# Kernel optimization log

Measured on AMD Instinct MI355X. Metric: run time of the kernel, lower is better.

Reference implementation:

```python
import math
import jax, jax.numpy as jnp
import numpy as np

B, N, CS, CZ, CH, H, PQ, PV = 1, 4096, 512, 128, 64, 16, 4, 8
BQ, BK = 32, 128
NB = N // BQ
CZ4 = CZ // 4
INF = 100000.0
EPS = 1e-8


def quat_to_rot(q):
    w, x, y, z = q[..., 0], q[..., 1], q[..., 2], q[..., 3]
    return jnp.stack([
        jnp.stack([1 - 2 * (y * y + z * z), 2 * (x * y - w * z), 2 * (x * z + w * y)], -1),
        jnp.stack([2 * (x * y + w * z), 1 - 2 * (x * x + z * z), 2 * (y * z - w * x)], -1),
        jnp.stack([2 * (x * z - w * y), 2 * (y * z + w * x), 1 - 2 * (x * x + y * y)], -1),
    ], -2)


def setup_inputs() -> dict:
    key = jax.random.key(0)
    ks = jax.random.split(key, 16)
    s = jax.random.normal(ks[0], (B, N, CS), jnp.float32)
    z = jax.random.normal(ks[1], (B, NB, BQ, BK, CZ), jnp.float32)
    trans = jax.random.normal(ks[2], (B, N, 3), jnp.float32) * 10.0
    quat = jax.random.normal(ks[3], (B, N, 4), jnp.float32)
    quat = quat / jnp.linalg.norm(quat, axis=-1, keepdims=True)
    rots = quat_to_rot(quat)
    s_mask = jnp.ones((B, N), jnp.float32)
    pad = (BK - BQ) // 2  # key window centered on each query block
    key_idx = (jnp.arange(NB)[:, None] * BQ - pad + jnp.arange(BK)[None, :]).astype(jnp.int32)

    def w(k, shp):
        return jax.random.normal(k, shp, jnp.float32) * (1.0 / math.sqrt(shp[0]))

    return {
        's': s, 'z': z, 'trans': trans, 'rots': rots, 's_mask': s_mask, 'key_idx': key_idx,
        'Wq': w(ks[4], (CS, H * CH)), 'Wk': w(ks[5], (CS, H * CH)), 'Wv': w(ks[6], (CS, H * CH)),
        'Wqp': w(ks[7], (CS, H * PQ * 3)), 'Wkvp': w(ks[8], (CS, H * (PQ + PV) * 3)),
        'Wb': w(ks[9], (CZ, H)), 'Wdz': w(ks[10], (CZ, CZ4)),
        'head_weights': jnp.full((H,), float(np.log(np.e - 1.0)), jnp.float32),  # softplus^-1(1)
        'Wout': w(ks[11], (H * (CZ4 + CH + PV * 4), CS)),
        'g_s': jnp.ones((CS,), jnp.float32), 'b_s': jnp.zeros((CS,), jnp.float32),
        'g_z': jnp.ones((CZ,), jnp.float32), 'b_z': jnp.zeros((CZ,), jnp.float32),
    }


def _ln(x, g, b):
    m = jnp.mean(x, -1, keepdims=True)
    v = jnp.mean((x - m) ** 2, -1, keepdims=True)
    return (x - m) * jax.lax.rsqrt(v + 1e-5) * g + b


def _ipa(s, z, trans, rots, s_mask, key_idx, Wq, Wk, Wv, Wqp, Wkvp, Wb, Wdz,
         head_weights, Wout, g_s, b_s, g_z, b_z):
    s_n = _ln(s, g_s, b_s)
    z_n = _ln(z, g_z, b_z)

    valid = (key_idx >= 0) & (key_idx < N)            # [NB, BK]
    idx = jnp.clip(key_idx, 0, N - 1)
    vf = valid.astype(s.dtype)[None]                  # [1, NB, BK]

    def gk(x):  # gather key window: [B,N,...] -> [B,NB,BK,...]
        return x[:, idx]

    sq = s_n.reshape(B, NB, BQ, CS)
    sk = gk(s_n) * vf[..., None]                      # zero-pad out-of-range keys

    tq = trans.reshape(B, NB, BQ, 3)
    rq = rots.reshape(B, NB, BQ, 3, 3)
    tk = gk(trans) * vf[..., None]
    rk = jnp.where(valid[None, :, :, None, None], gk(rots), jnp.eye(3, dtype=rots.dtype))

    q = (sq @ Wq).reshape(B, NB, BQ, H, CH)
    k = (sk @ Wk).reshape(B, NB, BK, H, CH)
    v = (sk @ Wv).reshape(B, NB, BK, H, CH)

    q_pts = (sq @ Wqp).reshape(B, NB, BQ, H * PQ, 3)
    q_pts = jnp.einsum('bnqij,bnqpj->bnqpi', rq, q_pts) + tq[:, :, :, None, :]
    q_pts = q_pts.reshape(B, NB, BQ, H, PQ, 3)

    kv_pts = (sk @ Wkvp).reshape(B, NB, BK, H * (PQ + PV), 3)
    kv_pts = jnp.einsum('bnkij,bnkpj->bnkpi', rk, kv_pts) + tk[:, :, :, None, :]
    kv_pts = kv_pts.reshape(B, NB, BK, H, PQ + PV, 3)
    k_pts, v_pts = kv_pts[..., :PQ, :], kv_pts[..., PQ:, :]

    bias = jnp.einsum('bnqkc,ch->bnqkh', z_n, Wb)
    a = jnp.einsum('bnqhc,bnkhc->bnqkh', q, k) * math.sqrt(1.0 / (3 * CH))
    a = a + math.sqrt(1.0 / 3) * bias

    disp = q_pts[:, :, :, None] - k_pts[:, :, None]   # [B,NB,BQ,BK,H,PQ,3]
    pt_att = jnp.sum(disp ** 2, -1)                   # [B,NB,BQ,BK,H,PQ]
    hw = jax.nn.softplus(head_weights) * math.sqrt(1.0 / (3 * (PQ * 9.0 / 2)))
    pt_att = -0.5 * jnp.sum(pt_att * hw[:, None], -1)  # [B,NB,BQ,BK,H]

    qm = s_mask.reshape(B, NB, BQ)
    km = gk(s_mask) * vf
    amask = INF * (qm[:, :, :, None] * km[:, :, None, :] - 1.0)

    a = a + pt_att + amask[..., None]
    a = jax.nn.softmax(jnp.swapaxes(a, -1, -2), axis=-1)  # [B,NB,BQ,H,BK]

    o = jnp.einsum('bnqhk,bnkhc->bnqhc', a, v).reshape(B, NB, BQ, H * CH)

    o_pt = jnp.einsum('bnqhk,bnkhpc->bnqhpc', a, v_pts)
    o_pt = jnp.einsum('bnqji,bnqhpj->bnqhpi', rq, o_pt - tq[:, :, :, None, None, :])
    o_pt_norm = jnp.sqrt(jnp.sum(o_pt ** 2, -1) + EPS).reshape(B, NB, BQ, H * PV)
    o_pt = o_pt.reshape(B, NB, BQ, H * PV * 3)

    pair_z = z_n @ Wdz                                # [B,NB,BQ,BK,CZ4]
    o_pair = jnp.einsum('bnqhk,bnqkc->bnqhc', a, pair_z).reshape(B, NB, BQ, H * CZ4)

    out = jnp.concatenate([o, o_pt, o_pt_norm, o_pair], -1) @ Wout
    return out.reshape(B, N, CS)


def reference(s, z, trans, rots, s_mask, key_idx, Wq, Wk, Wv, Wqp, Wkvp, Wb, Wdz,
              head_weights, Wout, g_s, b_s, g_z, b_z):
    return _ipa(s, z, trans, rots, s_mask, key_idx, Wq, Wk, Wv, Wqp, Wkvp, Wb, Wdz,
                head_weights, Wout, g_s, b_s, g_z, b_z)
```

## Files before the change

kernel.cpp:

```cpp
#include <hip/hip_runtime.h>
#include <math.h>

#define D_N 4096
#define PBW 3072
#define PPW 768
#define OFFK 1024
#define OFFV 2048
#define CATW 2048

typedef __bf16 bf16_t;
typedef __bf16 bf16x8 __attribute__((ext_vector_type(8)));
typedef __bf16 bf16x4 __attribute__((ext_vector_type(4)));
typedef float f32x4 __attribute__((ext_vector_type(4)));

__device__ __forceinline__ void gld16(const void* g, void* l) {
    __builtin_amdgcn_global_load_lds((const __attribute__((address_space(1))) unsigned int*)g,
                                     (__attribute__((address_space(3))) unsigned int*)l, 16, 0, 0);
}

__global__ __launch_bounds__(256) void k_prep(
    const float* __restrict__ Wq, const float* __restrict__ Wk, const float* __restrict__ Wv,
    const float* __restrict__ Wqp, const float* __restrict__ Wkvp, const float* __restrict__ Wout,
    const float* __restrict__ Wb, const float* __restrict__ Wdz,
    const float* __restrict__ gz, const float* __restrict__ bz,
    const float* __restrict__ s, const float* __restrict__ g_s, const float* __restrict__ b_s,
    bf16_t* __restrict__ wcatT, bf16_t* __restrict__ WoutT,
    bf16_t* __restrict__ WzT, float* __restrict__ Kv, bf16_t* __restrict__ s_nb)
{
    __shared__ float T[64][65];
    const int bx = blockIdx.x;
    const int tid = threadIdx.x;
    if (bx < 736) {
        const float* src; int ld, coff, r0;
        bf16_t* dst; int Rdst;
        if (bx < 480) {
            int c0 = (bx % 60) * 64;
            r0 = (bx / 60) * 64;
            if (c0 < 1024)      { src = Wq;   ld = 1024; coff = c0; }
            else if (c0 < 2048) { src = Wk;   ld = 1024; coff = c0 - 1024; }
            else if (c0 < 3072) { src = Wv;   ld = 1024; coff = c0 - 2048; }
            else if (c0 < 3264) { src = Wqp;  ld = 192;  coff = c0 - 3072; }
            else                { src = Wkvp; ld = 576;  coff = c0 - 3264; }
            dst = wcatT + (size_t)c0 * 512; Rdst = 512;
        } else {
            int b = bx - 480;
            int c0 = (b & 7) * 64;
            r0 = (b >> 3) * 64;
            src = Wout; ld = 512; coff = c0;
            dst = WoutT + (size_t)c0 * 2048; Rdst = 2048;
        }
        {
            int rr = tid >> 2, cb = (tid & 3) * 16;
            const float* p = src + (size_t)(r0 + rr) * ld + coff + cb;
            #pragma unroll
            for (int i = 0; i < 4; ++i)
                *(float4*)&T[rr][cb + i * 4] = *(const float4*)(p + i * 4);
        }
        __syncthreads();
        {
            int cc = tid >> 2, rb = (tid & 3) * 16;
            bf16_t* o = dst + (size_t)cc * Rdst + r0 + rb;
            bf16x8 o0, o1;
            #pragma unroll
            for (int j = 0; j < 8; ++j) o0[j] = (bf16_t)T[rb + j][cc];
            #pragma unroll
            for (int j = 0; j < 8; ++j) o1[j] = (bf16_t)T[rb + 8 + j][cc];
            *(bf16x8*)(o) = o0;
            *(bf16x8*)(o + 8) = o1;
        }
    } else if (bx == 736) {
        for (int i = tid; i < 6144; i += 256) {
            int j = i >> 7, c = i & 127;
            float w = (j < 16) ? Wb[c * 16 + j] : Wdz[c * 32 + (j - 16)];
            WzT[i] = (bf16_t)(gz[c] * w);
        }
        if (tid < 48) {
            int j = tid;
            float acc = 0.f;
            for (int c = 0; c < 128; ++c) {
                float w = (j < 16) ? Wb[c * 16 + j] : Wdz[c * 32 + (j - 16)];
                acc += bz[c] * w;
            }
            Kv[j] = acc;
        }
    } else {
        int row = (bx - 737) * 4 + (tid >> 6);
        int lane = tid & 63;
        const float4* p = (const float4*)(s + (size_t)row * 512);
        float4 v0 = p[lane];
        float4 v1 = p[lane + 64];
        float sum = v0.x + v0.y + v0.z + v0.w + v1.x + v1.y + v1.z + v1.w;
        float sq  = v0.x*v0.x + v0.y*v0.y + v0.z*v0.z + v0.w*v0.w
                  + v1.x*v1.x + v1.y*v1.y + v1.z*v1.z + v1.w*v1.w;
        #pragma unroll
        for (int off = 1; off < 64; off <<= 1) {
            sum += __shfl_xor(sum, off);
            sq  += __shfl_xor(sq, off);
        }
        float m = sum * (1.0f / 512.0f);
        float var = sq * (1.0f / 512.0f) - m * m;
        float rs = rsqrtf(var + 1e-5f);
        int c = lane * 4;
        int c2 = 256 + lane * 4;
        bf16x4 r0, r1;
        r0[0] = (bf16_t)((v0.x - m) * rs * g_s[c+0] + b_s[c+0]);
        r0[1] = (bf16_t)((v0.y - m) * rs * g_s[c+1] + b_s[c+1]);
        r0[2] = (bf16_t)((v0.z - m) * rs * g_s[c+2] + b_s[c+2]);
        r0[3] = (bf16_t)((v0.w - m) * rs * g_s[c+3] + b_s[c+3]);
        r1[0] = (bf16_t)((v1.x - m) * rs * g_s[c2+0] + b_s[c2+0]);
        r1[1] = (bf16_t)((v1.y - m) * rs * g_s[c2+1] + b_s[c2+1]);
        r1[2] = (bf16_t)((v1.z - m) * rs * g_s[c2+2] + b_s[c2+2]);
        r1[3] = (bf16_t)((v1.w - m) * rs * g_s[c2+3] + b_s[c2+3]);
        *(bf16x4*)(s_nb + (size_t)row * 512 + c)  = r0;
        *(bf16x4*)(s_nb + (size_t)row * 512 + c2) = r1;
    }
}

__global__ __launch_bounds__(256) void k_fused(
    const bf16_t* __restrict__ A, const bf16_t* __restrict__ BT,
    bf16_t* __restrict__ projb, float* __restrict__ projp,
    const float* __restrict__ z, const bf16_t* __restrict__ WzT, const float* __restrict__ Kv,
    float* __restrict__ biasT, bf16_t* __restrict__ pzT)
{
    __shared__ __align__(16) char smem[65536];
    const int bx = blockIdx.x;
    const int tid = threadIdx.x, lane = tid & 63, w = tid >> 6;
    int gemm_id = -1, zid = 0;
    if (bx < 2880) {
        int s3 = bx % 3, b3 = bx / 3;
        if (s3 == 0) gemm_id = b3;
        else         zid = b3 * 2 + s3 - 1;
    } else {
        zid = 1920 + (bx - 2880);
    }

    if (gemm_id >= 0) {
        bf16_t (*Asl)[32] = (bf16_t(*)[32])smem;
        bf16_t (*Bsl)[32] = (bf16_t(*)[32])(smem + 8192);
        const int row0 = (gemm_id / 30) * 128, col0 = (gemm_id % 30) * 128;
        const int wr = (w >> 1) * 64, wc = (w & 1) * 64;
        const int K = 512;
        const int sr = lane >> 2, k8 = (lane & 3) * 8;
        const bf16_t* Ab = A + (size_t)(row0 + w * 32 + sr) * K + k8;
        const bf16_t* Bb = BT + (size_t)(col0 + w * 32 + sr) * K + k8;
        f32x4 acc[4][4];
        #pragma unroll
        for (int m = 0; m < 4; ++m)
            #pragma unroll
            for (int n = 0; n < 4; ++n) acc[m][n] = (f32x4){0.f,0.f,0.f,0.f};
        for (int k0 = 0; k0 < K; k0 += 32) {
            __syncthreads();
            gld16(Ab + k0,          &Asl[w * 32][0]);
            gld16(Ab + k0 + 16 * K, &Asl[w * 32 + 16][0]);
            gld16(Bb + k0,          &Bsl[w * 32][0]);
            gld16(Bb + k0 + 16 * K, &Bsl[w * 32 + 16][0]);
            __syncthreads();
            bf16x8 af[4], bfr[4];
            #pragma unroll
            for (int m = 0; m < 4; ++m) af[m]  = *(const bf16x8*)&Asl[wr + m*16 + (lane & 15)][(lane >> 4) * 8];
            #pragma unroll
            for (int n = 0; n < 4; ++n) bfr[n] = *(const bf16x8*)&Bsl[wc + n*16 + (lane & 15)][(lane >> 4) * 8];
            #pragma unroll
            for (int m = 0; m < 4; ++m)
                #pragma unroll
                for (int n = 0; n < 4; ++n)
                    acc[m][n] = __builtin_amdgcn_mfma_f32_16x16x32_bf16(af[m], bfr[n], acc[m][n], 0, 0, 0);
        }
        if (col0 < 3072) {
            #pragma unroll
            for (int m = 0; m < 4; ++m)
                #pragma unroll
                for (int n = 0; n < 4; ++n)
                    #pragma unroll
                    for (int i = 0; i < 4; ++i)
                        projb[(size_t)(row0 + wr + m*16 + (lane >> 4)*4 + i) * PBW + col0 + wc + n*16 + (lane & 15)]
                            = (bf16_t)acc[m][n][i];
        } else {
            #pragma unroll
            for (int m = 0; m < 4; ++m)
                #pragma unroll
                for (int n = 0; n < 4; ++n)
                    #pragma unroll
                    for (int i = 0; i < 4; ++i)
                        projp[(size_t)(row0 + wr + m*16 + (lane >> 4)*4 + i) * PPW + col0 - 3072 + wc + n*16 + (lane & 15)]
                            = acc[m][n][i];
        }
        return;
    }

    float (*zbuf)[64][128] = (float(*)[64][128])smem;
    const int r16 = lane & 15, kg = lane >> 4;
    bf16x8 bfz[3][4];
    #pragma unroll
    for (int nt = 0; nt < 3; ++nt)
        #pragma unroll
        for (int kc = 0; kc < 4; ++kc)
            bfz[nt][kc] = *(const bf16x8*)(WzT + (size_t)(nt * 16 + r16) * 128 + kc * 32 + kg * 8);
    float K0 = Kv[r16], K1 = Kv[16 + r16], K2 = Kv[32 + r16];
    asm volatile("s_waitcnt vmcnt(0)" ::: "memory");
    __builtin_amdgcn_sched_barrier(0);

    const int gid = zid * 4 + w;
    const char* zb = (const char*)z + (size_t)gid * 64 * 512;
    char* lb0 = (char*)&zbuf[0][w * 16][0];
    char* lb1 = (char*)&zbuf[1][w * 16][0];

#define STAGE(i, lb) { \
    const char* gp_ = zb + (size_t)(i) * 8192 + lane * 16; \
    _Pragma("unroll") \
    for (int c_ = 0; c_ < 8; ++c_) gld16(gp_ + c_ * 1024, (lb) + c_ * 1024); }

#define PROCESS(i, b) { \
    const float* rp = &zbuf[b][w * 16 + r16][kg * 8]; \
    float4 za[4], zc[4]; \
    float sum = 0.f, sq = 0.f; \
    _Pragma("unroll") \
    for (int kc = 0; kc < 4; ++kc) { \
        float4 a_ = *(const float4*)(rp + kc * 32); \
        float4 b_ = *(const float4*)(rp + kc * 32 + 4); \
        za[kc] = a_; zc[kc] = b_; \
        sum += a_.x + a_.y + a_.z + a_.w + b_.x + b_.y + b_.z + b_.w; \
        sq  += a_.x*a_.x + a_.y*a_.y + a_.z*a_.z + a_.w*a_.w + b_.x*b_.x + b_.y*b_.y + b_.z*b_.z + b_.w*b_.w; \
    } \
    sum += __shfl_xor(sum, 16); sq += __shfl_xor(sq, 16); \
    sum += __shfl_xor(sum, 32); sq += __shfl_xor(sq, 32); \
    float m_ = sum * (1.0f / 128.0f); \
    float rs_ = rsqrtf(sq * (1.0f / 128.0f) - m_ * m_ + 1e-5f); \
    bf16x8 af[4]; \
    _Pragma("unroll") \
    for (int kc = 0; kc < 4; ++kc) { \
        af[kc][0] = (bf16_t)((za[kc].x - m_) * rs_); \
        af[kc][1] = (bf16_t)((za[kc].y - m_) * rs_); \
        af[kc][2] = (bf16_t)((za[kc].z - m_) * rs_); \
        af[kc][3] = (bf16_t)((za[kc].w - m_) * rs_); \
        af[kc][4] = (bf16_t)((zc[kc].x - m_) * rs_); \
        af[kc][5] = (bf16_t)((zc[kc].y - m_) * rs_); \
        af[kc][6] = (bf16_t)((zc[kc].z - m_) * rs_); \
        af[kc][7] = (bf16_t)((zc[kc].w - m_) * rs_); \
    } \
    f32x4 acc0 = (f32x4){0.f,0.f,0.f,0.f}; \
    f32x4 acc1 = (f32x4){0.f,0.f,0.f,0.f}; \
    f32x4 acc2 = (f32x4){0.f,0.f,0.f,0.f}; \
    _Pragma("unroll") \
    for (int kc = 0; kc < 4; ++kc) { \
        acc0 = __builtin_amdgcn_mfma_f32_16x16x32_bf16(af[kc], bfz[0][kc], acc0, 0, 0, 0); \
        acc1 = __builtin_amdgcn_mfma_f32_16x16x32_bf16(af[kc], bfz[1][kc], acc1, 0, 0, 0); \
        acc2 = __builtin_amdgcn_mfma_f32_16x16x32_bf16(af[kc], bfz[2][kc], acc2, 0, 0, 0); \
    } \
    const int t_ = gid * 4 + (i); \
    const int rowq_ = t_ >> 3; \
    const int k0_ = ((t_ & 7) << 4) + kg * 4; \
    float4 bw = {acc0[0] + K0, acc0[1] + K0, acc0[2] + K0, acc0[3] + K0}; \
    *(float4*)&biasT[((size_t)rowq_ * 16 + r16) * 128 + k0_] = bw; \
    bf16x4 p1, p2; \
    _Pragma("unroll") \
    for (int i2 = 0; i2 < 4; ++i2) { p1[i2] = (bf16_t)(acc1[i2] + K1); p2[i2] = (bf16_t)(acc2[i2] + K2); } \
    *(bf16x4*)&pzT[((size_t)rowq_ * 32 + r16) * 128 + k0_] = p1; \
    *(bf16x4*)&pzT[((size_t)rowq_ * 32 + 16 + r16) * 128 + k0_] = p2; }

#define LDS_DRAIN asm volatile("s_waitcnt lgkmcnt(0)" ::: "memory"); __builtin_amdgcn_sched_barrier(0);

    STAGE(0, lb0);
    STAGE(1, lb1);
    asm volatile("s_waitcnt vmcnt(8)" ::: "memory");
    __builtin_amdgcn_sched_barrier(0);
    PROCESS(0, 0);
    LDS_DRAIN
    STAGE(2, lb0);
    asm volatile("s_waitcnt vmcnt(8)" ::: "memory");
    __builtin_amdgcn_sched_barrier(0);
    PROCESS(1, 1);
    LDS_DRAIN
    STAGE(3, lb1);
    asm volatile("s_waitcnt vmcnt(8)" ::: "memory");
    __builtin_amdgcn_sched_barrier(0);
    PROCESS(2, 0);
    asm volatile("s_waitcnt vmcnt(0)" ::: "memory");
    __builtin_amdgcn_sched_barrier(0);
    PROCESS(3, 1);
#undef STAGE
#undef PROCESS
#undef LDS_DRAIN
}

__global__ __launch_bounds__(256) void k_attn4(
    const bf16_t* __restrict__ projb, const float* __restrict__ projp,
    const float* __restrict__ biasT, const float* __restrict__ rots,
    const float* __restrict__ trans, const float* __restrict__ smask,
    const int* __restrict__ kidx, const float* __restrict__ hwraw,
    bf16_t* __restrict__ catb, bf16_t* __restrict__ Pbf)
{
    __shared__ __align__(16) char pool[51840];
    bf16_t (*Qs)[72]   = (bf16_t(*)[72])pool;
    bf16_t (*Ks)[72]   = (bf16_t(*)[72])(pool + 32 * 72 * 2);
    bf16_t (*Vt)[136]  = (bf16_t(*)[136])pool;
    float  (*att)[132] = (float(*)[132])(pool + 26112);
    bf16_t (*Ps)[136]  = (bf16_t(*)[136])(pool + 26112);
    float  (*optmp)[33]= (float(*)[33])(pool + 26112 + 8704);
    float  (*kp_s)[12] = (float(*)[12])(pool + 43008);
    float  (*qp_s)[12] = (float(*)[12])(pool + 49152);
    float*  km_s       = (float*)(pool + 50688);
    float*  qm_s       = (float*)(pool + 51200);
    int*    rows_s     = (int*)(pool + 51328);

    const int wgid = blockIdx.x;
    const int swz = (wgid & 7) * 256 + (wgid >> 3);
    const int h = swz >> 7;
    const int nblk = swz & 127;
    const int tid = threadIdx.x;
    const int lane = tid & 63;
    const int w = tid >> 6;
    const int rowq0 = nblk * 32;
    const float hw = log1pf(__expf(hwraw[h])) * 0.13608276348795434f;

    if (tid < 128) {
        int ki = kidx[nblk * 128 + tid];
        int valid = (ki >= 0 && ki < D_N);
        int rr = ki < 0 ? 0 : (ki > D_N - 1 ? D_N - 1 : ki);
        rows_s[tid] = rr;
        km_s[tid] = valid ? smask[rr] : 0.0f;
    } else if (tid < 160) {
        qm_s[tid - 128] = smask[rowq0 + tid - 128];
    }
    __syncthreads();
    {
        int q = tid >> 3, cg = (tid & 7) * 8;
        *(bf16x8*)&Qs[q][cg] = *(const bf16x8*)(projb + (size_t)(rowq0 + q) * PBW + h * 64 + cg);
    }
    float Rk[9], tk0 = 0.f, tk1 = 0.f, tk2 = 0.f;
    if (tid < 128) {
        int rr = rows_s[tid];
        const float* Rp = rots + (size_t)rr * 9;
        const float* tp = trans + (size_t)rr * 3;
        #pragma unroll
        for (int e = 0; e < 9; ++e) Rk[e] = Rp[e];
        tk0 = tp[0]; tk1 = tp[1]; tk2 = tp[2];
        const float* kp = projp + (size_t)rr * PPW + 192 + h * 36;
        float4 p0 = *(const float4*)kp;
        float4 p1 = *(const float4*)(kp + 4);
        float4 p2 = *(const float4*)(kp + 8);
        float xs[4] = {p0.x, p0.w, p1.z, p2.y};
        float ys[4] = {p0.y, p1.x, p1.w, p2.z};
        float zs[4] = {p0.z, p1.y, p2.x, p2.w};
        #pragma unroll
        for (int p = 0; p < 4; ++p) {
            kp_s[tid][p*3+0] = Rk[0]*xs[p] + Rk[1]*ys[p] + Rk[2]*zs[p] + tk0;
            kp_s[tid][p*3+1] = Rk[3]*xs[p] + Rk[4]*ys[p] + Rk[5]*zs[p] + tk1;
            kp_s[tid][p*3+2] = Rk[6]*xs[p] + Rk[7]*ys[p] + Rk[8]*zs[p] + tk2;
        }
    } else {
        int j = tid - 128;
        {
            int q = j >> 2, p = j & 3;
            const float* Rp = rots + (size_t)(rowq0 + q) * 9;
            const float* tp = trans + (size_t)(rowq0 + q) * 3;
            const float* qp = projp + (size_t)(rowq0 + q) * PPW + h * 12 + p * 3;
            float x = qp[0], y = qp[1], zc = qp[2];
            qp_s[q][p*3+0] = Rp[0]*x + Rp[1]*y + Rp[2]*zc + tp[0];
            qp_s[q][p*3+1] = Rp[3]*x + Rp[4]*y + Rp[5]*zc + tp[1];
            qp_s[q][p*3+2] = Rp[6]*x + Rp[7]*y + Rp[8]*zc + tp[2];
        }
        {
            const bf16_t* pK = projb + (size_t)rows_s[j] * PBW + OFFK + h * 64;
            #pragma unroll
            for (int u = 0; u < 8; ++u)
                *(bf16x8*)&Ks[j][u * 8] = *(const bf16x8*)(pK + u * 8);
        }
    }
    __syncthreads();
    {
        #pragma unroll
        for (int j = 0; j < 4; ++j) {
            int T = w * 4 + j;
            int m = T & 1, n = T >> 1;
            f32x4 acc = (f32x4){0.f,0.f,0.f,0.f};
            #pragma unroll
            for (int kc = 0; kc < 2; ++kc) {
                bf16x8 a = *(const bf16x8*)&Qs[m*16 + (lane & 15)][kc*32 + (lane >> 4) * 8];
                bf16x8 b = *(const bf16x8*)&Ks[n*16 + (lane & 15)][kc*32 + (lane >> 4) * 8];
                acc = __builtin_amdgcn_mfma_f32_16x16x32_bf16(a, b, acc, 0, 0, 0);
            }
            #pragma unroll
            for (int i = 0; i < 4; ++i)
                att[m*16 + (lane >> 4)*4 + i][n*16 + (lane & 15)] = acc[i];
        }
    }
    __syncthreads();
    if (tid < 128) {
        const float* vp = projp + (size_t)rows_s[tid] * PPW + 192 + h * 36 + 12;
        float4 a0 = *(const float4*)(vp);
        float4 a1 = *(const float4*)(vp + 4);
        float4 a2 = *(const float4*)(vp + 8);
        float4 a3 = *(const float4*)(vp + 12);
        float4 a4 = *(const float4*)(vp + 16);
        float4 a5 = *(const float4*)(vp + 20);
        float xs[8] = {a0.x, a0.w, a1.z, a2.y, a3.x, a3.w, a4.z, a5.y};
        float ys[8] = {a0.y, a1.x, a1.w, a2.z, a3.y, a4.x, a4.w, a5.z};
        float zs[8] = {a0.z, a1.y, a2.x, a2.w, a3.z, a4.y, a5.x, a5.w};
        #pragma unroll
        for (int p = 0; p < 8; ++p) {
            Vt[64 + p*3 + 0][tid] = (bf16_t)(Rk[0]*xs[p] + Rk[1]*ys[p] + Rk[2]*zs[p] + tk0);
            Vt[64 + p*3 + 1][tid] = (bf16_t)(Rk[3]*xs[p] + Rk[4]*ys[p] + Rk[5]*zs[p] + tk1);
            Vt[64 + p*3 + 2][tid] = (bf16_t)(Rk[6]*xs[p] + Rk[7]*ys[p] + Rk[8]*zs[p] + tk2);
        }
        {
            bf16x8 zz = {};
            *(bf16x8*)&Vt[88 + (tid & 7)][(tid >> 3) * 8] = zz;
        }
    } else {
        int krow = tid - 128;
        const bf16_t* p = projb + (size_t)rows_s[krow] * PBW + OFFV + h * 64;
        #pragma unroll
        for (int u4 = 0; u4 < 8; ++u4) {
            bf16x8 v = *(const bf16x8*)(p + u4 * 8);
            #pragma unroll
            for (int jj = 0; jj < 8; ++jj) Vt[u4 * 8 + jj][krow] = v[jj];
        }
    }
    {
        int q = tid >> 3, kg = tid & 7;
        float qp[12];
        #pragma unroll
        for (int e = 0; e < 12; ++e) qp[e] = qp_s[q][e];
        float qm = qm_s[q];
        const float* bT = biasT + ((size_t)(rowq0 + q) * 16 + h) * 128;
        #pragma unroll
        for (int j2 = 0; j2 < 16; ++j2) {
            int k = kg + j2 * 8;
            float4 k0 = *(const float4*)&kp_s[k][0];
            float4 k1 = *(const float4*)&kp_s[k][4];
            float4 k2 = *(const float4*)&kp_s[k][8];
            float d0 = qp[0]-k0.x, d1 = qp[1]-k0.y, d2_ = qp[2]-k0.z, d3 = qp[3]-k0.w;
            float d4 = qp[4]-k1.x, d5 = qp[5]-k1.y, d6 = qp[6]-k1.z, d7 = qp[7]-k1.w;
            float d8 = qp[8]-k2.x, d9 = qp[9]-k2.y, d10 = qp[10]-k2.z, d11 = qp[11]-k2.w;
            float dd = d0*d0+d1*d1+d2_*d2_+d3*d3+d4*d4+d5*d5+d6*d6+d7*d7+d8*d8+d9*d9+d10*d10+d11*d11;
            float val = att[q][k] * 0.07216878364870323f
                      + 0.5773502691896258f * bT[k]
                      + 100000.0f * (qm * km_s[k] - 1.0f)
                      - 0.5f * hw * dd;
            att[q][k] = val;
        }
    }
    __syncthreads();
    {
        int q = tid >> 3, kg = tid & 7;
        float l[16];
        #pragma unroll
        for (int j2 = 0; j2 < 16; ++j2) l[j2] = att[q][kg + j2 * 8];
        float mx = l[0];
        #pragma unroll
        for (int j2 = 1; j2 < 16; ++j2) mx = fmaxf(mx, l[j2]);
        mx = fmaxf(mx, __shfl_xor(mx, 1));
        mx = fmaxf(mx, __shfl_xor(mx, 2));
        mx = fmaxf(mx, __shfl_xor(mx, 4));
        float se = 0.f;
        #pragma unroll
        for (int j2 = 0; j2 < 16; ++j2) { l[j2] = __expf(l[j2] - mx); se += l[j2]; }
        se += __shfl_xor(se, 1);
        se += __shfl_xor(se, 2);
        se += __shfl_xor(se, 4);
        float inv = 1.0f / se;
        __syncthreads();
        bf16_t* pg = Pbf + ((size_t)(rowq0 + q) * 16 + h) * 128;
        #pragma unroll
        for (int j2 = 0; j2 < 16; ++j2) {
            bf16_t pb = (bf16_t)(l[j2] * inv);
            Ps[q][kg + j2 * 8] = pb;
            pg[kg + j2 * 8] = pb;
        }
    }
    __syncthreads();
    {
        #pragma unroll
        for (int j = 0; j < 3; ++j) {
            int T = w * 3 + j;
            int m = T & 1, n = T >> 1;
            f32x4 acc = (f32x4){0.f,0.f,0.f,0.f};
            #pragma unroll
            for (int kc = 0; kc < 4; ++kc) {
                bf16x8 a = *(const bf16x8*)&Ps[m*16 + (lane & 15)][kc*32 + (lane >> 4) * 8];
                bf16x8 b = *(const bf16x8*)&Vt[n*16 + (lane & 15)][kc*32 + (lane >> 4) * 8];
                acc = __builtin_amdgcn_mfma_f32_16x16x32_bf16(a, b, acc, 0, 0, 0);
            }
            int rowb = m * 16 + (lane >> 4) * 4;
            int col = lane & 15;
            if (n < 4) {
                #pragma unroll
                for (int i = 0; i < 4; ++i)
                    catb[(size_t)(rowq0 + rowb + i) * CATW + h * 64 + n * 16 + col] = (bf16_t)acc[i];
            } else {
                #pragma unroll
                for (int i = 0; i < 4; ++i)
                    optmp[rowb + i][(n - 4) * 16 + col] = acc[i];
            }
        }
    }
    __syncthreads();
    {
        int q = tid >> 3, pp = tid & 7;
        float sx = optmp[q][pp * 3 + 0];
        float sy = optmp[q][pp * 3 + 1];
        float sz = optmp[q][pp * 3 + 2];
        const float* R = rots + (size_t)(rowq0 + q) * 9;
        const float* t = trans + (size_t)(rowq0 + q) * 3;
        float x = sx - t[0], y = sy - t[1], z2 = sz - t[2];
        float ox = R[0] * x + R[3] * y + R[6] * z2;
        float oy = R[1] * x + R[4] * y + R[7] * z2;
        float oz = R[2] * x + R[5] * y + R[8] * z2;
        bf16_t* cp = catb + (size_t)(rowq0 + q) * CATW;
        cp[1024 + h * 24 + pp * 3 + 0] = (bf16_t)ox;
        cp[1024 + h * 24 + pp * 3 + 1] = (bf16_t)oy;
        cp[1024 + h * 24 + pp * 3 + 2] = (bf16_t)oz;
        cp[1408 + h * 8 + pp] = (bf16_t)sqrtf(ox * ox + oy * oy + oz * oz + 1e-8f);
    }
}

__global__ __launch_bounds__(256) void k_opair(const bf16_t* __restrict__ Pbf,
    const bf16_t* __restrict__ pzT, bf16_t* __restrict__ catb)
{
    int tid = threadIdx.x, lane = tid & 63, w = tid >> 6;
    size_t rowq = (size_t)blockIdx.x * 4 + w;
    const bf16_t* Pp = Pbf + rowq * 2048;
    const bf16_t* zp = pzT + rowq * 4096;
    bf16x8 pa[4];
    #pragma unroll
    for (int kc = 0; kc < 4; ++kc)
        pa[kc] = *(const bf16x8*)(Pp + (size_t)(lane & 15) * 128 + kc * 32 + (lane >> 4) * 8);
    #pragma unroll
    for (int ct = 0; ct < 2; ++ct) {
        f32x4 acc = (f32x4){0.f,0.f,0.f,0.f};
        #pragma unroll
        for (int kc = 0; kc < 4; ++kc) {
            bf16x8 b = *(const bf16x8*)(zp + (size_t)(ct * 16 + (lane & 15)) * 128 + kc * 32 + (lane >> 4) * 8);
            acc = __builtin_amdgcn_mfma_f32_16x16x32_bf16(pa[kc], b, acc, 0, 0, 0);
        }
        #pragma unroll
        for (int i = 0; i < 4; ++i) {
            int hh = (lane >> 4) * 4 + i;
            catb[rowq * CATW + 1536 + hh * 32 + ct * 16 + (lane & 15)] = (bf16_t)acc[i];
        }
    }
}

__global__ __launch_bounds__(256) void gemm_out(const bf16_t* __restrict__ A, const bf16_t* __restrict__ BT,
    float* __restrict__ C)
{
    __shared__ bf16_t Asl[64][32];
    __shared__ bf16_t Bsl[128][32];
    const int tid = threadIdx.x, lane = tid & 63, w = tid >> 6;
    const int row0 = blockIdx.y * 64, col0 = blockIdx.x * 128;
    const int wr = (w >> 1) * 32, wc = (w & 1) * 64;
    const int K = 2048;
    const int sr = lane >> 2, k8 = (lane & 3) * 8;
    const bf16_t* Ab = A + (size_t)(row0 + w * 16 + sr) * K + k8;
    const bf16_t* Bb = BT + (size_t)(col0 + w * 32 + sr) * K + k8;
    f32x4 acc[2][4];
    #pragma unroll
    for (int m = 0; m < 2; ++m)
        #pragma unroll
        for (int n = 0; n < 4; ++n) acc[m][n] = (f32x4){0.f,0.f,0.f,0.f};
    for (int k0 = 0; k0 < K; k0 += 32) {
        __syncthreads();
        gld16(Ab + k0,          &Asl[w * 16][0]);
        gld16(Bb + k0,          &Bsl[w * 32][0]);
        gld16(Bb + k0 + 16 * K, &Bsl[w * 32 + 16][0]);
        __syncthreads();
        bf16x8 af[2], bfr[4];
        #pragma unroll
        for (int m = 0; m < 2; ++m) af[m]  = *(const bf16x8*)&Asl[wr + m*16 + (lane & 15)][(lane >> 4) * 8];
        #pragma unroll
        for (int n = 0; n < 4; ++n) bfr[n] = *(const bf16x8*)&Bsl[wc + n*16 + (lane & 15)][(lane >> 4) * 8];
        #pragma unroll
        for (int m = 0; m < 2; ++m)
            #pragma unroll
            for (int n = 0; n < 4; ++n)
                acc[m][n] = __builtin_amdgcn_mfma_f32_16x16x32_bf16(af[m], bfr[n], acc[m][n], 0, 0, 0);
    }
    #pragma unroll
    for (int m = 0; m < 2; ++m)
        #pragma unroll
        for (int n = 0; n < 4; ++n)
            #pragma unroll
            for (int i = 0; i < 4; ++i)
                C[(size_t)(row0 + wr + m*16 + (lane >> 4)*4 + i) * 512 + col0 + wc + n*16 + (lane & 15)] = acc[m][n][i];
}

extern "C" void kernel_launch(void* const* d_in, const int* in_sizes, int n_in,
                              void* d_out, int out_size, void* d_ws, size_t ws_size,
                              hipStream_t stream)
{
    (void)in_sizes; (void)n_in; (void)out_size;
    const float* s     = (const float*)d_in[0];
    const float* z     = (const float*)d_in[1];
    const float* trans = (const float*)d_in[2];
    const float* rots  = (const float*)d_in[3];
    const float* smask = (const float*)d_in[4];
    const int*   kidx  = (const int*)d_in[5];
    const float* Wq    = (const float*)d_in[6];
    const float* Wk    = (const float*)d_in[7];
    const float* Wv    = (const float*)d_in[8];
    const float* Wqp   = (const float*)d_in[9];
    const float* Wkvp  = (const float*)d_in[10];
    const float* Wb    = (const float*)d_in[11];
    const float* Wdz   = (const float*)d_in[12];
    const float* hw    = (const float*)d_in[13];
    const float* Wout  = (const float*)d_in[14];
    const float* g_s   = (const float*)d_in[15];
    const float* b_s   = (const float*)d_in[16];
    const float* g_z   = (const float*)d_in[17];
    const float* b_z   = (const float*)d_in[18];

    char* ws = (char*)d_ws;
    bf16_t* projb = (bf16_t*)(ws);
    float*  projp = (float*)(ws + 25165824);
    float*  biasT = (float*)(ws + 37748736);
    bf16_t* wcatT = (bf16_t*)(ws + 71303168);
    bf16_t* s_nb  = (bf16_t*)(ws + 75235328);
    bf16_t* pzT   = (bf16_t*)(ws + 79429632);
    bf16_t* Pbf   = (bf16_t*)(ws + 112984064);
    bf16_t* catb  = (bf16_t*)(ws + 129761280);
    bf16_t* WoutT = (bf16_t*)(ws + 146538496);
    bf16_t* WzT   = (bf16_t*)(ws + 148635648);
    float*  Kv    = (float*)(ws + 148647936);
    if (ws_size < (size_t)148648128) return;
    float* out = (float*)d_out;

    k_prep<<<1761, 256, 0, stream>>>(Wq, Wk, Wv, Wqp, Wkvp, Wout, Wb, Wdz, g_z, b_z,
                                     s, g_s, b_s, wcatT, WoutT, WzT, Kv, s_nb);
    k_fused<<<3008, 256, 0, stream>>>(s_nb, wcatT, projb, projp, z, WzT, Kv, biasT, pzT);
    k_attn4<<<2048, 256, 0, stream>>>(projb, projp, biasT, rots, trans, smask, kidx, hw, catb, Pbf);
    k_opair<<<1024, 256, 0, stream>>>(Pbf, pzT, catb);
    gemm_out<<<dim3(4, 64), 256, 0, stream>>>(catb, WoutT, out);
}
```

Measured before the change: 222.6 us.

## Load z directly from global in fused kernel, dropping LDS double-buffering

After: 210.6 us. 5.4% less time.

```diff
diff --git a/kernel.cpp b/kernel.cpp
--- a/kernel.cpp
+++ b/kernel.cpp
@@ -122,7 +122,8 @@
     const float* __restrict__ z, const bf16_t* __restrict__ WzT, const float* __restrict__ Kv,
     float* __restrict__ biasT, bf16_t* __restrict__ pzT)
 {
-    __shared__ __align__(16) char smem[65536];
+    __shared__ bf16_t Asl[128][32];
+    __shared__ bf16_t Bsl[128][32];
     const int bx = blockIdx.x;
     const int tid = threadIdx.x, lane = tid & 63, w = tid >> 6;
     int gemm_id = -1, zid = 0;
@@ -135,8 +136,6 @@
     }
 
     if (gemm_id >= 0) {
-        bf16_t (*Asl)[32] = (bf16_t(*)[32])smem;
-        bf16_t (*Bsl)[32] = (bf16_t(*)[32])(smem + 8192);
         const int row0 = (gemm_id / 30) * 128, col0 = (gemm_id % 30) * 128;
         const int wr = (w >> 1) * 64, wc = (w & 1) * 64;
         const int K = 512;
@@ -188,7 +187,6 @@
         return;
     }
 
-    float (*zbuf)[64][128] = (float(*)[64][128])smem;
     const int r16 = lane & 15, kg = lane >> 4;
     bf16x8 bfz[3][4];
     #pragma unroll
@@ -196,91 +194,58 @@
         #pragma unroll
         for (int kc = 0; kc < 4; ++kc)
             bfz[nt][kc] = *(const bf16x8*)(WzT + (size_t)(nt * 16 + r16) * 128 + kc * 32 + kg * 8);
-    float K0 = Kv[r16], K1 = Kv[16 + r16], K2 = Kv[32 + r16];
-    asm volatile("s_waitcnt vmcnt(0)" ::: "memory");
-    __builtin_amdgcn_sched_barrier(0);
-
+    const float K0 = Kv[r16], K1 = Kv[16 + r16], K2 = Kv[32 + r16];
     const int gid = zid * 4 + w;
-    const char* zb = (const char*)z + (size_t)gid * 64 * 512;
-    char* lb0 = (char*)&zbuf[0][w * 16][0];
-    char* lb1 = (char*)&zbuf[1][w * 16][0];
-
-#define STAGE(i, lb) { \
-    const char* gp_ = zb + (size_t)(i) * 8192 + lane * 16; \
-    _Pragma("unroll") \
-    for (int c_ = 0; c_ < 8; ++c_) gld16(gp_ + c_ * 1024, (lb) + c_ * 1024); }
-
-#define PROCESS(i, b) { \
-    const float* rp = &zbuf[b][w * 16 + r16][kg * 8]; \
-    float4 za[4], zc[4]; \
-    float sum = 0.f, sq = 0.f; \
-    _Pragma("unroll") \
-    for (int kc = 0; kc < 4; ++kc) { \
-        float4 a_ = *(const float4*)(rp + kc * 32); \
-        float4 b_ = *(const float4*)(rp + kc * 32 + 4); \
-        za[kc] = a_; zc[kc] = b_; \
-        sum += a_.x + a_.y + a_.z + a_.w + b_.x + b_.y + b_.z + b_.w; \
-        sq  += a_.x*a_.x + a_.y*a_.y + a_.z*a_.z + a_.w*a_.w + b_.x*b_.x + b_.y*b_.y + b_.z*b_.z + b_.w*b_.w; \
-    } \
-    sum += __shfl_xor(sum, 16); sq += __shfl_xor(sq, 16); \
-    sum += __shfl_xor(sum, 32); sq += __shfl_xor(sq, 32); \
-    float m_ = sum * (1.0f / 128.0f); \
-    float rs_ = rsqrtf(sq * (1.0f / 128.0f) - m_ * m_ + 1e-5f); \
-    bf16x8 af[4]; \
-    _Pragma("unroll") \
-    for (int kc = 0; kc < 4; ++kc) { \
-        af[kc][0] = (bf16_t)((za[kc].x - m_) * rs_); \
-        af[kc][1] = (bf16_t)((za[kc].y - m_) * rs_); \
-        af[kc][2] = (bf16_t)((za[kc].z - m_) * rs_); \
-        af[kc][3] = (bf16_t)((za[kc].w - m_) * rs_); \
-        af[kc][4] = (bf16_t)((zc[kc].x - m_) * rs_); \
-        af[kc][5] = (bf16_t)((zc[kc].y - m_) * rs_); \
-        af[kc][6] = (bf16_t)((zc[kc].z - m_) * rs_); \
-        af[kc][7] = (bf16_t)((zc[kc].w - m_) * rs_); \
-    } \
-    f32x4 acc0 = (f32x4){0.f,0.f,0.f,0.f}; \
-    f32x4 acc1 = (f32x4){0.f,0.f,0.f,0.f}; \
-    f32x4 acc2 = (f32x4){0.f,0.f,0.f,0.f}; \
-    _Pragma("unroll") \
-    for (int kc = 0; kc < 4; ++kc) { \
-        acc0 = __builtin_amdgcn_mfma_f32_16x16x32_bf16(af[kc], bfz[0][kc], acc0, 0, 0, 0); \
-        acc1 = __builtin_amdgcn_mfma_f32_16x16x32_bf16(af[kc], bfz[1][kc], acc1, 0, 0, 0); \
-        acc2 = __builtin_amdgcn_mfma_f32_16x16x32_bf16(af[kc], bfz[2][kc], acc2, 0, 0, 0); \
-    } \
-    const int t_ = gid * 4 + (i); \
-    const int rowq_ = t_ >> 3; \
-    const int k0_ = ((t_ & 7) << 4) + kg * 4; \
-    float4 bw = {acc0[0] + K0, acc0[1] + K0, acc0[2] + K0, acc0[3] + K0}; \
-    *(float4*)&biasT[((size_t)rowq_ * 16 + r16) * 128 + k0_] = bw; \
-    bf16x4 p1, p2; \
-    _Pragma("unroll") \
-    for (int i2 = 0; i2 < 4; ++i2) { p1[i2] = (bf16_t)(acc1[i2] + K1); p2[i2] = (bf16_t)(acc2[i2] + K2); } \
-    *(bf16x4*)&pzT[((size_t)rowq_ * 32 + r16) * 128 + k0_] = p1; \
-    *(bf16x4*)&pzT[((size_t)rowq_ * 32 + 16 + r16) * 128 + k0_] = p2; }
-
-#define LDS_DRAIN asm volatile("s_waitcnt lgkmcnt(0)" ::: "memory"); __builtin_amdgcn_sched_barrier(0);
-
-    STAGE(0, lb0);
-    STAGE(1, lb1);
-    asm volatile("s_waitcnt vmcnt(8)" ::: "memory");
-    __builtin_amdgcn_sched_barrier(0);
-    PROCESS(0, 0);
-    LDS_DRAIN
-    STAGE(2, lb0);
-    asm volatile("s_waitcnt vmcnt(8)" ::: "memory");
-    __builtin_amdgcn_sched_barrier(0);
-    PROCESS(1, 1);
-    LDS_DRAIN
-    STAGE(3, lb1);
-    asm volatile("s_waitcnt vmcnt(8)" ::: "memory");
-    __builtin_amdgcn_sched_barrier(0);
-    PROCESS(2, 0);
-    asm volatile("s_waitcnt vmcnt(0)" ::: "memory");
-    __builtin_amdgcn_sched_barrier(0);
-    PROCESS(3, 1);
-#undef STAGE
-#undef PROCESS
-#undef LDS_DRAIN
+
+    #pragma unroll 2
+    for (int it = 0; it < 4; ++it) {
+        const int t_ = gid * 4 + it;
+        const float* zp = z + ((size_t)t_ * 16 + r16) * 128 + kg * 8;
+        float4 za[4], zc[4];
+        float sum = 0.f, sq = 0.f;
+        #pragma unroll
+        for (int kc = 0; kc < 4; ++kc) {
+            za[kc] = *(const float4*)(zp + kc * 32);
+            zc[kc] = *(const float4*)(zp + kc * 32 + 4);
+            sum += za[kc].x + za[kc].y + za[kc].z + za[kc].w + zc[kc].x + zc[kc].y + zc[kc].z + zc[kc].w;
+            sq  += za[kc].x*za[kc].x + za[kc].y*za[kc].y + za[kc].z*za[kc].z + za[kc].w*za[kc].w
+                 + zc[kc].x*zc[kc].x + zc[kc].y*zc[kc].y + zc[kc].z*zc[kc].z + zc[kc].w*zc[kc].w;
+        }
+        sum += __shfl_xor(sum, 16); sq += __shfl_xor(sq, 16);
+        sum += __shfl_xor(sum, 32); sq += __shfl_xor(sq, 32);
+        float m_ = sum * (1.0f / 128.0f);
+        float rs_ = rsqrtf(sq * (1.0f / 128.0f) - m_ * m_ + 1e-5f);
+        bf16x8 af[4];
+        #pragma unroll
+        for (int kc = 0; kc < 4; ++kc) {
+            af[kc][0] = (bf16_t)((za[kc].x - m_) * rs_);
+            af[kc][1] = (bf16_t)((za[kc].y - m_) * rs_);
+            af[kc][2] = (bf16_t)((za[kc].z - m_) * rs_);
+            af[kc][3] = (bf16_t)((za[kc].w - m_) * rs_);
+            af[kc][4] = (bf16_t)((zc[kc].x - m_) * rs_);
+            af[kc][5] = (bf16_t)((zc[kc].y - m_) * rs_);
+            af[kc][6] = (bf16_t)((zc[kc].z - m_) * rs_);
+            af[kc][7] = (bf16_t)((zc[kc].w - m_) * rs_);
+        }
+        f32x4 acc0 = (f32x4){0.f,0.f,0.f,0.f};
+        f32x4 acc1 = (f32x4){0.f,0.f,0.f,0.f};
+        f32x4 acc2 = (f32x4){0.f,0.f,0.f,0.f};
+        #pragma unroll
+        for (int kc = 0; kc < 4; ++kc) {
+            acc0 = __builtin_amdgcn_mfma_f32_16x16x32_bf16(af[kc], bfz[0][kc], acc0, 0, 0, 0);
+            acc1 = __builtin_amdgcn_mfma_f32_16x16x32_bf16(af[kc], bfz[1][kc], acc1, 0, 0, 0);
+            acc2 = __builtin_amdgcn_mfma_f32_16x16x32_bf16(af[kc], bfz[2][kc], acc2, 0, 0, 0);
+        }
+        const int rowq_ = t_ >> 3;
+        const int k0_ = ((t_ & 7) << 4) + kg * 4;
+        float4 bw = {acc0[0] + K0, acc0[1] + K0, acc0[2] + K0, acc0[3] + K0};
+        *(float4*)&biasT[((size_t)rowq_ * 16 + r16) * 128 + k0_] = bw;
+        bf16x4 p1, p2;
+        #pragma unroll
+        for (int i2 = 0; i2 < 4; ++i2) { p1[i2] = (bf16_t)(acc1[i2] + K1); p2[i2] = (bf16_t)(acc2[i2] + K2); }
+        *(bf16x4*)&pzT[((size_t)rowq_ * 32 + r16) * 128 + k0_] = p1;
+        *(bf16x4*)&pzT[((size_t)rowq_ * 32 + 16 + r16) * 128 + k0_] = p2;
+    }
 }
 
 __global__ __launch_bounds__(256) void k_attn4(
```
